# Kernel optimization log

Hardware: AMD Instinct MI355X
Metric: run time of the kernel (lower is better)

The kernel has to match this reference:

```python
import jax, jax.numpy as jnp
import numpy as np

N, K, D = 32768, 8192, 64


def setup_inputs() -> dict:
    key = jax.random.key(0)
    k1, k2, k3 = jax.random.split(key, 3)
    z = jax.random.normal(k1, (N, D), dtype=jnp.float32)
    # Riemannian sensitivity weight per sample (positive scalar from decoder VJP norms)
    g_weight = jax.random.uniform(k2, (N,), dtype=jnp.float32)
    # codebook: nn.Embedding(num_embeddings, embedding_dim), weight ~ N(0,1)
    embedding = jax.random.normal(k3, (K, D), dtype=jnp.float32)
    return {"z": z, "g_weight": g_weight, "embedding": embedding}


def reference(z, g_weight, embedding):
    # d(z, e) = ||z||^2 + ||e||^2 - 2 z e^T  -> [N, K]
    z_flat = z.reshape(-1, embedding.shape[1])
    distances = (
        jnp.sum(z_flat * z_flat, axis=1, keepdims=True)
        + jnp.sum(embedding * embedding, axis=1)
        - 2.0 * jnp.matmul(z_flat, embedding.T)
    )
    # Riemannian scaling: d_R = d * G(z)
    riemannian_distances = distances * g_weight[:, None]
    return jnp.argmin(riemannian_distances, axis=1)
```

## Files before the change

kernel.cpp:

```cpp
#include <hip/hip_runtime.h>
#include <hip/hip_fp16.h>
#include <cfloat>
#include <climits>


typedef short  s16x8  __attribute__((ext_vector_type(8)));
typedef float  f32x16 __attribute__((ext_vector_type(16)));

static constexpr int N_ = 32768;
static constexpr int K_ = 8192;
static constexpr int D_ = 64;
static constexpr int NTILES = K_ / 32;
static constexpr int REC_SLOTS = 576;
static constexpr size_t REC_BYTES = (size_t)NTILES * REC_SLOTS * 16;
static constexpr float FLAG_MARGIN = 0.001953125f;
static constexpr float RESID_SCALE = 1024.0f;
static constexpr float RESID_INV   = 0.0009765625f;

struct alignas(16) Part3 { float b1, b2; int i1, pad; };

__device__ __forceinline__ short f2h_s(float x) {
    __half h = __float2half(x);
    return (short)__half_as_short(h);
}

#define MFMA16(A, B, C) __builtin_amdgcn_mfma_f32_32x32x16_f16((A), (B), (C), 0, 0, 0)

__global__ void rq_prep(const float* __restrict__ emb, s16x8* __restrict__ recs)
{
    __shared__ double sp[32][8];
    const int tile = blockIdx.x;
    const int t = threadIdx.x;
    const int c = t >> 3, q = t & 7;
    const int f = q >> 1, h = q & 1;
    const float* src = emb + (size_t)(tile * 32 + c) * D_ + q * 8;
    float4 a = ((const float4*)src)[0];
    float4 b = ((const float4*)src)[1];
    float e[8] = {a.x, a.y, a.z, a.w, b.x, b.y, b.z, b.w};
    s16x8 u1, u2;
    double s = 0.0;
    #pragma unroll
    for (int j = 0; j < 8; ++j) {
        __half h1 = __float2half(e[j]);
        float r = e[j] - __half2float(h1);
        u1[j] = (short)__half_as_short(h1);
        u2[j] = f2h_s(r * RESID_SCALE);
        s = fma((double)e[j], (double)e[j], s);
    }
    const size_t rb = (size_t)tile * REC_SLOTS;
    recs[rb + f * 64 + h * 32 + c] = u1;
    recs[rb + 320 + f * 64 + h * 32 + c] = u2;
    sp[c][q] = s;
    __syncthreads();
    if (t < 32) {
        double se = 0.0;
        #pragma unroll
        for (int j = 0; j < 8; ++j) se += sp[t][j];
        se *= 0.5;
        float sf = (float)se;
        __half sh = __float2half(sf);
        float  sr = sf - __half2float(sh);
        s16x8 v;
        #pragma unroll
        for (int j = 0; j < 8; ++j) v[j] = 0;
        v[0] = (short)__half_as_short(sh);
        v[1] = f2h_s(sr);
        recs[rb + 256 + t] = v;
    } else if (t < 64) {
        s16x8 v;
        #pragma unroll
        for (int j = 0; j < 8; ++j) v[j] = 0;
        recs[rb + 256 + t] = v;
    }
}

__global__ __launch_bounds__(256)
void rq_main(const float* __restrict__ z,
             const s16x8* __restrict__ recs,
             Part3* __restrict__ parts,
             int tpb )
{
    const int tid  = threadIdx.x;
    const int wave = tid >> 6, lane = tid & 63;
    const int col  = lane & 31, h = lane >> 5;
    const int slice = blockIdx.y;
    const int tile0 = slice * tpb;
    const int rowbase = blockIdx.x * 256 + wave * 64;

    s16x8 zn1[2][4], zn2[2][4];
    #pragma unroll
    for (int g = 0; g < 2; ++g) {
        const int zrow = rowbase + 32 * g + col;
        #pragma unroll
        for (int f = 0; f < 4; ++f) {
            const float* src = z + (size_t)zrow * D_ + f * 16 + h * 8;
            float4 a = ((const float4*)src)[0];
            float4 b = ((const float4*)src)[1];
            float e[8] = {a.x, a.y, a.z, a.w, b.x, b.y, b.z, b.w};
            #pragma unroll
            for (int j = 0; j < 8; ++j) {
                float zn = -e[j];
                __half h1 = __float2half(zn);
                zn1[g][f][j] = (short)__half_as_short(h1);
                zn2[g][f][j] = f2h_s((zn - __half2float(h1)) * RESID_SCALE);
            }
        }
    }
    s16x8 bse;
    #pragma unroll
    for (int j = 0; j < 8; ++j) bse[j] = 0;
    if (h == 0) { bse[0] = (short)0x3C00; bse[1] = (short)0x3C00; }

    f32x16 zacc;
    #pragma unroll
    for (int r = 0; r < 16; ++r) zacc[r] = 0.0f;

    float b1e[2] = {FLT_MAX, FLT_MAX}, b2e[2] = {FLT_MAX, FLT_MAX};
    float b1o[2] = {FLT_MAX, FLT_MAX}, b2o[2] = {FLT_MAX, FLT_MAX};
    int   i1e[2] = {INT_MAX, INT_MAX}, i1o[2] = {INT_MAX, INT_MAX};

    for (int t = 0; t < tpb; ++t) {
        const s16x8* gp = recs + (size_t)(tile0 + t) * REC_SLOTS;
        s16x8 ea[4], e2a[4], sea;
        #pragma unroll
        for (int f = 0; f < 4; ++f) ea[f]  = gp[f * 64 + lane];
        sea = gp[256 + lane];
        #pragma unroll
        for (int f = 0; f < 4; ++f) e2a[f] = gp[320 + f * 64 + lane];

        f32x16 accSE = MFMA16(sea, bse, zacc);

        const int tb32 = (tile0 + t) * 32;
        #pragma unroll
        for (int g = 0; g < 2; ++g) {
            f32x16 acc, acc2;
            acc  = MFMA16(ea[0],  zn1[g][0], accSE);
            acc2 = MFMA16(e2a[0], zn1[g][0], zacc);
            acc  = MFMA16(ea[1],  zn1[g][1], acc);
            acc2 = MFMA16(e2a[1], zn1[g][1], acc2);
            acc  = MFMA16(ea[2],  zn1[g][2], acc);
            acc2 = MFMA16(e2a[2], zn1[g][2], acc2);
            acc  = MFMA16(ea[3],  zn1[g][3], acc);
            acc2 = MFMA16(e2a[3], zn1[g][3], acc2);
            acc2 = MFMA16(ea[0],  zn2[g][0], acc2);
            acc2 = MFMA16(ea[1],  zn2[g][1], acc2);
            acc2 = MFMA16(ea[2],  zn2[g][2], acc2);
            acc2 = MFMA16(ea[3],  zn2[g][3], acc2);

            #pragma unroll
            for (int r = 0; r < 16; r += 2) {
                float v = fmaf(acc2[r], RESID_INV, acc[r]);
                int cru = tb32 + ((r & 3) + 8 * (r >> 2));
                b2e[g] = fminf(b2e[g], fmaxf(v, b1e[g]));
                bool lt = v < b1e[g];
                i1e[g] = lt ? cru : i1e[g];
                b1e[g] = fminf(b1e[g], v);
            }
            #pragma unroll
            for (int r = 1; r < 16; r += 2) {
                float v = fmaf(acc2[r], RESID_INV, acc[r]);
                int cru = tb32 + ((r & 3) + 8 * (r >> 2));
                b2o[g] = fminf(b2o[g], fmaxf(v, b1o[g]));
                bool lt = v < b1o[g];
                i1o[g] = lt ? cru : i1o[g];
                b1o[g] = fminf(b1o[g], v);
            }
        }
    }

    #pragma unroll
    for (int g = 0; g < 2; ++g) {
        float b1, b2; int i1;
        b2 = fminf(fminf(b2e[g], b2o[g]), fmaxf(b1e[g], b1o[g]));
        if (b1o[g] < b1e[g]) { b1 = b1o[g]; i1 = i1o[g]; } else { b1 = b1e[g]; i1 = i1e[g]; }
        i1 += 4 * h;

        float ob1 = __shfl_xor(b1, 32);
        float ob2 = __shfl_xor(b2, 32);
        int   oi1 = __shfl_xor(i1, 32);
        float nb2 = fminf(fminf(b2, ob2), fmaxf(b1, ob1));
        if (ob1 < b1) { b1 = ob1; i1 = oi1; }
        b2 = nb2;
        if (lane < 32) {
            Part3 p; p.b1 = b1; p.b2 = b2; p.i1 = i1; p.pad = 0;
            parts[(size_t)slice * N_ + (rowbase + 32 * g + lane)] = p;
        }
    }
}

__global__ void rq_merge(const Part3* __restrict__ parts,
                         const float* __restrict__ g,
                         int* __restrict__ out,
                         int* __restrict__ counter,
                         int* __restrict__ list,
                         int nsl, int maxf)
{
    int row = blockIdx.x * 256 + threadIdx.x;
    Part3 p = parts[row];
    float b1 = p.b1, b2 = p.b2; int i1 = p.i1;
    for (int s = 1; s < nsl; ++s) {
        Part3 q = parts[(size_t)s * N_ + row];
        float m2 = fminf(fminf(b2, q.b2), fmaxf(b1, q.b1));
        if (q.b1 < b1) { b1 = q.b1; i1 = q.i1; }
        b2 = m2;
    }
    if (g[row] == 0.0f) { out[row] = 0; return; }
    out[row] = i1;
    if (b2 - b1 < FLAG_MARGIN) {
        int idx = atomicAdd(counter, 1);
        if (idx < maxf) list[idx] = row;
    }
}

__global__ __launch_bounds__(256)
void rq_cleanup_part(const float* __restrict__ z,
                     const float* __restrict__ emb,
                     const int* __restrict__ counter,
                     const int* __restrict__ list,
                     double* __restrict__ vparts,
                     int* __restrict__ iparts,
                     int maxf)
{
    int cnt = *counter; if (cnt > maxf) cnt = maxf;
    const int jobs = cnt * 8;
    const int wid  = (blockIdx.x * 256 + threadIdx.x) >> 6;
    const int lane = threadIdx.x & 63;
    const int nw   = gridDim.x * 4;

    for (int j = wid; j < jobs; j += nw) {
        const int row = list[j >> 3];
        const int sl  = j & 7;
        float zr[64];
        {
            const float4* zp = reinterpret_cast<const float4*>(z + (size_t)row * D_);
            #pragma unroll
            for (int q = 0; q < 16; ++q) {
                float4 v = zp[q];
                zr[4*q] = v.x; zr[4*q+1] = v.y; zr[4*q+2] = v.z; zr[4*q+3] = v.w;
            }
        }
        double bv = DBL_MAX; int bi = INT_MAX;
        for (int i = 0; i < 16; ++i) {
            const int c = sl * 1024 + i * 64 + lane;
            const float4* ep = reinterpret_cast<const float4*>(emb + (size_t)c * D_);
            double sd0 = 0, sd1 = 0, sq0 = 0, sq1 = 0;
            #pragma unroll
            for (int q = 0; q < 16; ++q) {
                float4 ev = ep[q];
                sd0 = fma((double)ev.x, (double)zr[4*q+0], sd0);
                sq0 = fma((double)ev.x, (double)ev.x, sq0);
                sd1 = fma((double)ev.y, (double)zr[4*q+1], sd1);
                sq1 = fma((double)ev.y, (double)ev.y, sq1);
                sd0 = fma((double)ev.z, (double)zr[4*q+2], sd0);
                sq0 = fma((double)ev.z, (double)ev.z, sq0);
                sd1 = fma((double)ev.w, (double)zr[4*q+3], sd1);
                sq1 = fma((double)ev.w, (double)ev.w, sq1);
            }
            double v = 0.5 * (sq0 + sq1) - (sd0 + sd1);
            if (v < bv) { bv = v; bi = c; }
        }
        #pragma unroll
        for (int m = 1; m < 64; m <<= 1) {
            double ov = __shfl_xor(bv, m);
            int    oi = __shfl_xor(bi, m);
            if (ov < bv || (ov == bv && oi < bi)) { bv = ov; bi = oi; }
        }
        if (lane == 0) { vparts[j] = bv; iparts[j] = bi; }
    }
}

__global__ void rq_cleanup_fin(const int* __restrict__ counter,
                               const int* __restrict__ list,
                               const double* __restrict__ vparts,
                               const int* __restrict__ iparts,
                               int* __restrict__ out, int maxf)
{
    int cnt = *counter; if (cnt > maxf) cnt = maxf;
    int j = blockIdx.x * 256 + threadIdx.x;
    if (j >= cnt) return;
    double bv = vparts[j * 8]; int bi = iparts[j * 8];
    #pragma unroll
    for (int s = 1; s < 8; ++s) {
        double v = vparts[j * 8 + s]; int i = iparts[j * 8 + s];
        if (v < bv || (v == bv && i < bi)) { bv = v; bi = i; }
    }
    out[list[j]] = bi;
}

__global__ __launch_bounds__(256, 4)
void rq_fallback(const float* __restrict__ z,
                 const float* __restrict__ emb,
                 const float* __restrict__ g,
                 int* __restrict__ out)
{
    __shared__ float  lds_e[64][64];
    __shared__ double lds_se[64];
    const int tid = threadIdx.x;
    const int row = blockIdx.x * 256 + tid;
    float zr[64];
    {
        const float4* zp = reinterpret_cast<const float4*>(z + (size_t)row * D_);
        #pragma unroll
        for (int j = 0; j < 16; ++j) {
            float4 v = zp[j];
            zr[4*j] = v.x; zr[4*j+1] = v.y; zr[4*j+2] = v.z; zr[4*j+3] = v.w;
        }
    }
    float best32 = FLT_MAX; double bestv = DBL_MAX; int bestidx = 0;
    for (int t = 0; t < K_; t += 64) {
        __syncthreads();
        {
            const float4* src = reinterpret_cast<const float4*>(emb + (size_t)t * D_);
            float4* dst = reinterpret_cast<float4*>(&lds_e[0][0]);
            #pragma unroll
            for (int j = 0; j < 4; ++j) dst[tid + j * 256] = src[tid + j * 256];
        }
        if (tid < 64) {
            const float* er = emb + (size_t)(t + tid) * D_;
            double s = 0;
            for (int d = 0; d < 64; ++d) s = fma((double)er[d], (double)er[d], s);
            lds_se[tid] = 0.5 * s;
        }
        __syncthreads();
        float cv0 = FLT_MAX, cv1 = FLT_MAX, cv2 = FLT_MAX;
        int ck0 = 0, ck1 = 0, ck2 = 0;
        for (int kk = 0; kk < 64; ++kk) {
            const float4* ep = reinterpret_cast<const float4*>(&lds_e[kk][0]);
            float a0 = 0, a1 = 0, a2 = 0, a3 = 0;
            #pragma unroll
            for (int j = 0; j < 16; ++j) {
                float4 e4 = ep[j];
                a0 = fmaf(zr[4*j], e4.x, a0);   a1 = fmaf(zr[4*j+1], e4.y, a1);
                a2 = fmaf(zr[4*j+2], e4.z, a2); a3 = fmaf(zr[4*j+3], e4.w, a3);
            }
            float val = (float)lds_se[kk] - ((a0 + a1) + (a2 + a3));
            if (val < best32 + 0.0625f) {
                cv2 = cv1; ck2 = ck1; cv1 = cv0; ck1 = ck0;
                cv0 = val; ck0 = kk;
                best32 = fminf(best32, val);
            }
        }
        const float thr = best32 + 0.0625f;
        #pragma unroll
        for (int r = 0; r < 3; ++r) {
            float cv = (r == 0) ? cv2 : (r == 1) ? cv1 : cv0;
            int   ck = (r == 0) ? ck2 : (r == 1) ? ck1 : ck0;
            if (cv < thr) {
                const float4* ep = reinterpret_cast<const float4*>(&lds_e[ck][0]);
                double s0 = 0, s1 = 0, s2 = 0, s3 = 0;
                #pragma unroll
                for (int j = 0; j < 16; ++j) {
                    float4 e4 = ep[j];
                    s0 = fma((double)zr[4*j],   (double)e4.x, s0);
                    s1 = fma((double)zr[4*j+1], (double)e4.y, s1);
                    s2 = fma((double)zr[4*j+2], (double)e4.z, s2);
                    s3 = fma((double)zr[4*j+3], (double)e4.w, s3);
                }
                double vd = lds_se[ck] - ((s0 + s1) + (s2 + s3));
                int kidx = t + ck;
                if (vd < bestv) { bestv = vd; bestidx = kidx; }
                else if (vd == bestv && kidx < bestidx) bestidx = kidx;
            }
        }
    }
    out[row] = (g[row] == 0.0f) ? 0 : bestidx;
}

extern "C" void kernel_launch(void* const* d_in, const int* in_sizes, int n_in,
                              void* d_out, int out_size, void* d_ws, size_t ws_size,
                              hipStream_t stream)
{
    const float* z   = (const float*)d_in[0];
    const float* g   = (const float*)d_in[1];
    const float* emb = (const float*)d_in[2];
    int* out = (int*)d_out;

    auto need = [&](int s, int mf) {
        return REC_BYTES + (size_t)s * N_ * sizeof(Part3) + 64
             + (size_t)mf * 4 + (size_t)mf * 8 * 8 + (size_t)mf * 8 * 4;
    };
    int nsl = 0, maxf = 0;
    const int nsls[4]  = {8, 4, 2, 1};
    const int maxfs[2] = {16384, 2048};
    for (int a = 0; a < 4 && !nsl; ++a)
        for (int b = 0; b < 2; ++b)
            if (need(nsls[a], maxfs[b]) <= ws_size) { nsl = nsls[a]; maxf = maxfs[b]; break; }

    if (!nsl) {
        rq_fallback<<<N_ / 256, 256, 0, stream>>>(z, emb, g, out);
        return;
    }

    char* w = (char*)d_ws;
    s16x8*  recs    = (s16x8*)w;                              w += REC_BYTES;
    Part3*  parts   = (Part3*)w;                              w += (size_t)nsl * N_ * sizeof(Part3);
    int*    counter = (int*)w;                                w += 64;
    int*    list    = (int*)w;                                w += (size_t)maxf * 4;
    double* vparts  = (double*)w;                             w += (size_t)maxf * 8 * 8;
    int*    iparts  = (int*)w;

    rq_prep<<<NTILES, 256, 0, stream>>>(emb, recs);
    hipMemsetAsync(counter, 0, sizeof(int), stream);
    rq_main<<<dim3(N_ / 256, nsl), 256, 0, stream>>>(z, recs, parts, NTILES / nsl);
    rq_merge<<<N_ / 256, 256, 0, stream>>>(parts, g, out, counter, list, nsl, maxf);
    rq_cleanup_part<<<1024, 256, 0, stream>>>(z, emb, counter, list, vparts, iparts, maxf);
    rq_cleanup_fin<<<128, 256, 0, stream>>>(counter, list, vparts, iparts, out, maxf);
}
```

Before: 169.9 us.

## Double-buffer codebook tiles in LDS, merge argmin chains, fewer K slices

The main kernel now stages each codebook tile record in a double-buffered shared-memory array. The next tile is prefetched from global memory into registers while the MFMAs on the current tile run, so waves no longer each re-read the tile from global/L2. The even/odd split of the running top-2 tracking is merged into one chain, with an index tie-break in the cross-half reduction. The slice count drops from 8 to 4, which halves partial-result traffic at the cost of fewer blocks, and the counter memset is folded into the prep kernel. A __syncthreads per tile is added, and the single dependent min chain lengthens the serial ALU work.

```diff
diff --git a/kernel.cpp b/kernel.cpp
--- a/kernel.cpp
+++ b/kernel.cpp
@@ -26,11 +26,13 @@
 
 #define MFMA16(A, B, C) __builtin_amdgcn_mfma_f32_32x32x16_f16((A), (B), (C), 0, 0, 0)
 
-__global__ void rq_prep(const float* __restrict__ emb, s16x8* __restrict__ recs)
+__global__ void rq_prep(const float* __restrict__ emb, s16x8* __restrict__ recs,
+                        int* __restrict__ counter)
 {
     __shared__ double sp[32][8];
     const int tile = blockIdx.x;
     const int t = threadIdx.x;
+    if (tile == 0 && t == 0) *counter = 0;
     const int c = t >> 3, q = t & 7;
     const int f = q >> 1, h = q & 1;
     const float* src = emb + (size_t)(tile * 32 + c) * D_ + q * 8;
@@ -80,6 +82,7 @@
              Part3* __restrict__ parts,
              int tpb )
 {
+    __shared__ s16x8 lbuf[2][REC_SLOTS];
     const int tid  = threadIdx.x;
     const int wave = tid >> 6, lane = tid & 63;
     const int col  = lane & 31, h = lane >> 5;
@@ -115,22 +118,38 @@
     #pragma unroll
     for (int r = 0; r < 16; ++r) zacc[r] = 0.0f;
 
-    float b1e[2] = {FLT_MAX, FLT_MAX}, b2e[2] = {FLT_MAX, FLT_MAX};
-    float b1o[2] = {FLT_MAX, FLT_MAX}, b2o[2] = {FLT_MAX, FLT_MAX};
-    int   i1e[2] = {INT_MAX, INT_MAX}, i1o[2] = {INT_MAX, INT_MAX};
+    {
+        const size_t gb = (size_t)tile0 * REC_SLOTS;
+        lbuf[0][tid]       = recs[gb + tid];
+        lbuf[0][256 + tid] = recs[gb + 256 + tid];
+        if (tid < 64) lbuf[0][512 + tid] = recs[gb + 512 + tid];
+    }
+    __syncthreads();
+
+    float b1[2] = {FLT_MAX, FLT_MAX}, b2[2] = {FLT_MAX, FLT_MAX};
+    int   i1[2] = {INT_MAX, INT_MAX};
 
     for (int t = 0; t < tpb; ++t) {
-        const s16x8* gp = recs + (size_t)(tile0 + t) * REC_SLOTS;
+        const int cb = t & 1, nb = cb ^ 1;
+        const bool pf = (t + 1 < tpb);
+        s16x8 r0, r1, r2;
+        if (pf) {
+            const size_t gb = (size_t)(tile0 + t + 1) * REC_SLOTS;
+            r0 = recs[gb + tid];
+            r1 = recs[gb + 256 + tid];
+            if (tid < 64) r2 = recs[gb + 512 + tid];
+        }
+
         s16x8 ea[4], e2a[4], sea;
         #pragma unroll
-        for (int f = 0; f < 4; ++f) ea[f]  = gp[f * 64 + lane];
-        sea = gp[256 + lane];
-        #pragma unroll
-        for (int f = 0; f < 4; ++f) e2a[f] = gp[320 + f * 64 + lane];
+        for (int f = 0; f < 4; ++f) ea[f]  = lbuf[cb][f * 64 + lane];
+        sea = lbuf[cb][256 + lane];
+        #pragma unroll
+        for (int f = 0; f < 4; ++f) e2a[f] = lbuf[cb][320 + f * 64 + lane];
 
         f32x16 accSE = MFMA16(sea, bse, zacc);
 
-        const int tb32 = (tile0 + t) * 32;
+        const int cb32 = (tile0 + t) * 32 + 4 * h;
         #pragma unroll
         for (int g = 0; g < 2; ++g) {
             f32x16 acc, acc2;
@@ -148,41 +167,35 @@
             acc2 = MFMA16(ea[3],  zn2[g][3], acc2);
 
             #pragma unroll
-            for (int r = 0; r < 16; r += 2) {
+            for (int r = 0; r < 16; ++r) {
                 float v = fmaf(acc2[r], RESID_INV, acc[r]);
-                int cru = tb32 + ((r & 3) + 8 * (r >> 2));
-                b2e[g] = fminf(b2e[g], fmaxf(v, b1e[g]));
-                bool lt = v < b1e[g];
-                i1e[g] = lt ? cru : i1e[g];
-                b1e[g] = fminf(b1e[g], v);
-            }
-            #pragma unroll
-            for (int r = 1; r < 16; r += 2) {
-                float v = fmaf(acc2[r], RESID_INV, acc[r]);
-                int cru = tb32 + ((r & 3) + 8 * (r >> 2));
-                b2o[g] = fminf(b2o[g], fmaxf(v, b1o[g]));
-                bool lt = v < b1o[g];
-                i1o[g] = lt ? cru : i1o[g];
-                b1o[g] = fminf(b1o[g], v);
-            }
-        }
+                int cr = cb32 + (r & 3) + 8 * (r >> 2);
+                b2[g] = fminf(b2[g], fmaxf(v, b1[g]));
+                bool lt = v < b1[g];
+                i1[g] = lt ? cr : i1[g];
+                b1[g] = fminf(b1[g], v);
+            }
+        }
+
+        if (pf) {
+            lbuf[nb][tid]       = r0;
+            lbuf[nb][256 + tid] = r1;
+            if (tid < 64) lbuf[nb][512 + tid] = r2;
+        }
+        __syncthreads();
     }
 
     #pragma unroll
     for (int g = 0; g < 2; ++g) {
-        float b1, b2; int i1;
-        b2 = fminf(fminf(b2e[g], b2o[g]), fmaxf(b1e[g], b1o[g]));
-        if (b1o[g] < b1e[g]) { b1 = b1o[g]; i1 = i1o[g]; } else { b1 = b1e[g]; i1 = i1e[g]; }
-        i1 += 4 * h;
-
-        float ob1 = __shfl_xor(b1, 32);
-        float ob2 = __shfl_xor(b2, 32);
-        int   oi1 = __shfl_xor(i1, 32);
-        float nb2 = fminf(fminf(b2, ob2), fmaxf(b1, ob1));
-        if (ob1 < b1) { b1 = ob1; i1 = oi1; }
-        b2 = nb2;
+        float B1 = b1[g], B2 = b2[g]; int I1 = i1[g];
+        float ob1 = __shfl_xor(B1, 32);
+        float ob2 = __shfl_xor(B2, 32);
+        int   oi1 = __shfl_xor(I1, 32);
+        float nb2 = fminf(fminf(B2, ob2), fmaxf(B1, ob1));
+        if (ob1 < B1 || (ob1 == B1 && oi1 < I1)) { B1 = ob1; I1 = oi1; }
+        B2 = nb2;
         if (lane < 32) {
-            Part3 p; p.b1 = b1; p.b2 = b2; p.i1 = i1; p.pad = 0;
+            Part3 p; p.b1 = B1; p.b2 = B2; p.i1 = I1; p.pad = 0;
             parts[(size_t)slice * N_ + (rowbase + 32 * g + lane)] = p;
         }
     }
@@ -380,9 +393,9 @@
              + (size_t)mf * 4 + (size_t)mf * 8 * 8 + (size_t)mf * 8 * 4;
     };
     int nsl = 0, maxf = 0;
-    const int nsls[4]  = {8, 4, 2, 1};
+    const int nsls[3]  = {4, 2, 1};
     const int maxfs[2] = {16384, 2048};
-    for (int a = 0; a < 4 && !nsl; ++a)
+    for (int a = 0; a < 3 && !nsl; ++a)
         for (int b = 0; b < 2; ++b)
             if (need(nsls[a], maxfs[b]) <= ws_size) { nsl = nsls[a]; maxf = maxfs[b]; break; }
 
@@ -399,8 +412,7 @@
     double* vparts  = (double*)w;                             w += (size_t)maxf * 8 * 8;
     int*    iparts  = (int*)w;
 
-    rq_prep<<<NTILES, 256, 0, stream>>>(emb, recs);
-    hipMemsetAsync(counter, 0, sizeof(int), stream);
+    rq_prep<<<NTILES, 256, 0, stream>>>(emb, recs, counter);
     rq_main<<<dim3(N_ / 256, nsl), 256, 0, stream>>>(z, recs, parts, NTILES / nsl);
     rq_merge<<<N_ / 256, 256, 0, stream>>>(parts, g, out, counter, list, nsl, maxf);
     rq_cleanup_part<<<1024, 256, 0, stream>>>(z, emb, counter, list, vparts, iparts, maxf);
```

After: 164.5 us. -3.1%, faster.
